# Optimization experiments

Measured on AMD Instinct MI355X. Metric: run time of the kernel, lower is better.

Reference implementation:

```python
import jax, jax.numpy as jnp
import numpy as np

B, S, D, NH = 128, 1500, 128, 4
HD = D // NH          # 32
V = 4096
K = 4                 # causal conv kernel size
FF = 192              # round_up(1.3 * 128, 64) per xLSTM FeedForwardConfig
EPS = 1e-5
NEG = -1e30           # acts as -inf for the stabilizer state


def layer_norm(x, w):
    mu = jnp.mean(x, axis=-1, keepdims=True)
    var = jnp.mean((x - mu) ** 2, axis=-1, keepdims=True)
    return (x - mu) * jax.lax.rsqrt(var + EPS) * w


def _forward(seq, emb, conv_w, conv_b, Wi, Wf, Wz, Wo, Ri, Rf, Rz, Ro,
             bi, bf, bz, bo, gn_w, ln1_w, ln2_w, ffn_up, ffn_down, ln_post_w):
    x = emb[seq]                                   # (B,S,D) embedding (row 0 = pad)
    h = layer_norm(x, ln1_w)                       # pre-norm of sLSTM block
    # causal depthwise conv + SiLU feeds the i/f gate projections
    xc = jax.lax.conv_general_dilated(
        h, conv_w, window_strides=(1,), padding=[(K - 1, 0)],
        dimension_numbers=("NWC", "WIO", "NWC"), feature_group_count=D) + conv_b
    xc = jax.nn.silu(xc)

    def headproj(v, W):                            # block-diagonal per-head linear
        return jnp.einsum("bshd,hed->bshe", v.reshape(B, S, NH, HD), W)

    gi, gf = headproj(xc, Wi), headproj(xc, Wf)
    gz, go = headproj(h, Wz), headproj(h, Wo)
    gates = jnp.stack([gi, gf, gz, go], 0).transpose(2, 0, 1, 3, 4)  # (S,4,B,NH,HD)

    def step(carry, g):
        y, c, n, m = carry                         # each (B,NH,HD)
        ir = g[0] + jnp.einsum("bhd,hde->bhe", y, Ri) + bi
        fr = g[1] + jnp.einsum("bhd,hde->bhe", y, Rf) + bf
        zr = g[2] + jnp.einsum("bhd,hde->bhe", y, Rz) + bz
        orr = g[3] + jnp.einsum("bhd,hde->bhe", y, Ro) + bo
        logf = m + jax.nn.log_sigmoid(fr)          # stabilized exponential gating
        m_new = jnp.maximum(ir, logf)
        ig = jnp.exp(ir - m_new)
        fg = jnp.exp(logf - m_new)
        c_new = fg * c + ig * jnp.tanh(zr)
        n_new = fg * n + ig
        y_new = jax.nn.sigmoid(orr) * c_new / n_new
        return (y_new, c_new, n_new, m_new), y_new

    z0 = jnp.zeros((B, NH, HD), jnp.float32)
    m0 = jnp.full((B, NH, HD), NEG, jnp.float32)
    _, ys = jax.lax.scan(step, (z0, z0, z0, m0), gates)  # (S,B,NH,HD)

    y = ys.transpose(1, 0, 2, 3)                   # (B,S,NH,HD)
    mu = jnp.mean(y, axis=-1, keepdims=True)       # multi-head group norm
    var = jnp.mean((y - mu) ** 2, axis=-1, keepdims=True)
    y = (y - mu) * jax.lax.rsqrt(var + EPS) * gn_w.reshape(NH, HD)
    x = x + y.reshape(B, S, D)                     # residual

    h2 = layer_norm(x, ln2_w)                      # gated FFN (GEGLU-style, bias-free)
    u = h2 @ ffn_up                                # (B,S,2*FF)
    x = x + (jax.nn.gelu(u[..., :FF], approximate=False) * u[..., FF:]) @ ffn_down
    x = layer_norm(x, ln_post_w)                   # post-blocks LayerNorm
    return jnp.mean(x, axis=1)                     # mean pool -> (B,D)


def setup_inputs():
    key = jax.random.key(0)
    ks = jax.random.split(key, 24)
    sc = lambda k, shp, s=0.05: jax.random.normal(k, shp, jnp.float32) * s
    emb = sc(ks[0], (V, D), 0.1).at[0].set(0.0)    # padding_idx=0
    return {
        "seq": jax.random.randint(ks[1], (B, S), 0, V),
        "emb": emb,
        "conv_w": sc(ks[2], (K, 1, D), 0.1),
        "conv_b": sc(ks[3], (D,), 0.02),
        "Wi": sc(ks[4], (NH, HD, HD), 0.1),
        "Wf": sc(ks[5], (NH, HD, HD), 0.1),
        "Wz": sc(ks[6], (NH, HD, HD), 0.1),
        "Wo": sc(ks[7], (NH, HD, HD), 0.1),
        "Ri": sc(ks[8], (NH, HD, HD), 0.1),
        "Rf": sc(ks[9], (NH, HD, HD), 0.1),
        "Rz": sc(ks[10], (NH, HD, HD), 0.1),
        "Ro": sc(ks[11], (NH, HD, HD), 0.1),
        "bi": sc(ks[12], (NH, HD), 0.02),
        "bf": jnp.tile(jnp.linspace(3.0, 6.0, HD, dtype=jnp.float32), (NH, 1)),
        "bz": sc(ks[14], (NH, HD), 0.02),
        "bo": sc(ks[15], (NH, HD), 0.02),
        "gn_w": jnp.ones((D,), jnp.float32),
        "ln1_w": jnp.ones((D,), jnp.float32),
        "ln2_w": jnp.ones((D,), jnp.float32),
        "ffn_up": sc(ks[16], (D, 2 * FF), 0.08),
        "ffn_down": sc(ks[17], (FF, D), 0.08),
        "ln_post_w": jnp.ones((D,), jnp.float32),
    }


def reference(seq, emb, conv_w, conv_b, Wi, Wf, Wz, Wo, Ri, Rf, Rz, Ro,
              bi, bf, bz, bo, gn_w, ln1_w, ln2_w, ffn_up, ffn_down, ln_post_w):
    return _forward(seq, emb, conv_w, conv_b, Wi, Wf, Wz, Wo, Ri, Rf, Rz, Ro,
                    bi, bf, bz, bo, gn_w, ln1_w, ln2_w, ffn_up, ffn_down, ln_post_w)
```

## Files before the change

kernel.cpp:

```cpp
#include <hip/hip_runtime.h>
#include <hip/hip_bf16.h>
#include <math.h>

#define BB   128
#define SS   1500
#define DD   128
#define NHH  4
#define HDD  32
#define FFF  192
#define EPSV 1e-5f
#define GXCH 16

typedef __bf16   bf16x8 __attribute__((ext_vector_type(8)));
typedef float    f32x4  __attribute__((ext_vector_type(4)));
typedef float    f32x2  __attribute__((ext_vector_type(2)));
typedef _Float16 f16x2  __attribute__((ext_vector_type(2)));

__global__ void __launch_bounds__(256) k_stats(
    const int* __restrict__ seq, const float* __restrict__ emb,
    float* __restrict__ stats)
{
    const int w = threadIdx.x >> 6, l = threadIdx.x & 63;
    for (int t = blockIdx.x * 4 + w; t < BB * SS; t += gridDim.x * 4) {
        int tok = seq[t];
        f32x2 v = *(const f32x2*)(emb + (size_t)tok * DD + 2 * l);
        float s1 = v[0] + v[1], s2 = v[0] * v[0] + v[1] * v[1];
        #pragma unroll
        for (int mm = 1; mm <= 32; mm <<= 1) {
            s1 += __shfl_xor(s1, mm);
            s2 += __shfl_xor(s2, mm);
        }
        if (l == 0) {
            float mu  = s1 * (1.f / 128.f);
            float var = s2 * (1.f / 128.f) - mu * mu;
            stats[2 * t]     = mu;
            stats[2 * t + 1] = rsqrtf(var + EPSV);
        }
    }
}

__global__ void k_prep(const float* __restrict__ up, const float* __restrict__ down,
                       const float* __restrict__ Ri, const float* __restrict__ Rf,
                       const float* __restrict__ Rz, const float* __restrict__ Ro,
                       __bf16* __restrict__ wupT, __bf16* __restrict__ wdnT,
                       float* __restrict__ rtA, float* __restrict__ rtB)
{
    int i = blockIdx.x * 256 + threadIdx.x;
    if (i < 384 * 128) {
        int n = i >> 7, k = i & 127;
        wupT[i] = (__bf16)up[k * 384 + n];
    }
    int j = i - 384 * 128;
    if (j >= 0 && j < 128 * 192) {
        int n = j / 192, k = j - n * 192;
        wdnT[j] = (__bf16)down[k * 128 + n];
    }
    int kx = i - (384 * 128 + 128 * 192);
    if (kx >= 0 && kx < 8192) {
        int h = kx >> 11, upq = (kx >> 10) & 1, e = (kx >> 5) & 31, d = kx & 31;
        int src = h * 1024 + d * 32 + e;
        rtA[kx] = upq ? Rz[src] : Ri[src];
        rtB[kx] = upq ? Ro[src] : Rf[src];
    }
}

__global__ void __launch_bounds__(256, 2) k_gx(
    const int* __restrict__ seq, const float* __restrict__ emb,
    const float* __restrict__ stats,
    const float* __restrict__ convw, const float* __restrict__ convb,
    const float* __restrict__ ln1w,
    const float* __restrict__ Wi, const float* __restrict__ Wf,
    const float* __restrict__ Wz, const float* __restrict__ Wo,
    const float* __restrict__ bi, const float* __restrict__ bfv,
    const float* __restrict__ bz, const float* __restrict__ bo,
    unsigned int* __restrict__ gx)
{
    __shared__ float hl[(GXCH + 3) * 128];
    __shared__ float xcl[4 * 32];

    const int tid = threadIdx.x;
    const int w   = tid >> 6;
    const int l   = tid & 63;
    const int p   = l >> 5;
    const int e   = l & 31;
    const int b   = blockIdx.y;
    const int s0  = blockIdx.x * GXCH;
    const int ch  = w * 32 + e;

    const float* W0 = p ? Wf : Wi;
    const float* W1 = p ? Wo : Wz;
    float wr0[32], wr1[32];
    #pragma unroll
    for (int q = 0; q < 32; ++q) {
        wr0[q] = W0[w * 1024 + e * 32 + q];
        wr1[q] = W1[w * 1024 + e * 32 + q];
    }
    #pragma unroll
    for (int q = 0; q < 32; ++q) {
        asm volatile("" : "+v"(wr0[q]));
        asm volatile("" : "+v"(wr1[q]));
    }
    const float b0 = (p ? bfv : bi)[w * 32 + e];
    const float b1 = (p ? bo  : bz)[w * 32 + e];
    const float cb = convb[ch];
    float cw[4];
    #pragma unroll
    for (int k = 0; k < 4; ++k) cw[k] = convw[k * DD + ch];

    for (int idx = tid; idx < (GXCH + 3) * 128; idx += 256) {
        int r = idx >> 7, d = idx & 127;
        int sg = s0 - 3 + r;
        float hv = 0.f;
        if (sg >= 0 && sg < SS) {
            int tok = seq[b * SS + sg];
            float mu = stats[2 * (b * SS + sg)];
            float rs = stats[2 * (b * SS + sg) + 1];
            hv = (emb[(size_t)tok * DD + d] - mu) * rs * ln1w[d];
        }
        hl[idx] = hv;
    }
    __syncthreads();

    for (int t = 0; t < GXCH; ++t) {
        if (s0 + t >= SS) break;
        float xc = cb;
        #pragma unroll
        for (int k = 0; k < 4; ++k) xc = fmaf(hl[(t + k) * 128 + ch], cw[k], xc);
        xc = xc * __builtin_amdgcn_rcpf(1.f + __expf(-xc));
        if (l < 32) xcl[w * 32 + e] = xc;

        const f32x4* xs = (const f32x4*)(xcl + w * 32);
        const f32x4* hs = (const f32x4*)(hl + (t + 3) * 128 + w * 32);

        float a0 = b0, a1 = 0.f, c0 = b1, c1 = 0.f;
        #pragma unroll
        for (int q8 = 0; q8 < 8; q8 += 2) {
            f32x4 xv0 = xs[q8], xv1 = xs[q8 + 1];
            f32x4 hv0 = hs[q8], hv1 = hs[q8 + 1];
            #pragma unroll
            for (int j = 0; j < 4; ++j) {
                a0 = fmaf(xv0[j], wr0[4 * q8 + j],     a0);
                a1 = fmaf(xv1[j], wr0[4 * q8 + 4 + j], a1);
                c0 = fmaf(hv0[j], wr1[4 * q8 + j],     c0);
                c1 = fmaf(hv1[j], wr1[4 * q8 + 4 + j], c1);
            }
        }
        float a = a0 + a1;
        float cz = c0 + c1;

        float ap = __shfl_xor(a, 32);
        float cp = __shfl_xor(cz, 32);
        if (l < 32) {
            f16x2 w0; w0[0] = (_Float16)a;  w0[1] = (_Float16)ap;
            f16x2 w1; w1[0] = (_Float16)cz; w1[1] = (_Float16)cp;
            size_t base = ((size_t)(b * 4 + w) * SS + s0 + t) * 64;
            gx[base + l]      = __builtin_bit_cast(unsigned int, w0);
            gx[base + 32 + l] = __builtin_bit_cast(unsigned int, w1);
        }
    }
}

__global__ void __launch_bounds__(64, 1)
__attribute__((amdgpu_waves_per_eu(1)))
k_scan2(
    const unsigned int* __restrict__ gx,
    const float* __restrict__ rtA, const float* __restrict__ rtB,
    _Float16* __restrict__ yout)
{
    const int l  = threadIdx.x;
    const int up = l >> 5;
    const int e  = l & 31;
    const int bh = blockIdx.x;
    const int b  = bh >> 2, h = bh & 3;

    const float* pa = rtA + ((size_t)((h * 2 + up) * 32 + e) * 32);
    const float* pb = rtB + ((size_t)((h * 2 + up) * 32 + e) * 32);
    f32x4 A0 = *(const f32x4*)(pa +  0), A1 = *(const f32x4*)(pa +  4);
    f32x4 A2 = *(const f32x4*)(pa +  8), A3 = *(const f32x4*)(pa + 12);
    f32x4 A4 = *(const f32x4*)(pa + 16), A5 = *(const f32x4*)(pa + 20);
    f32x4 A6 = *(const f32x4*)(pa + 24), A7 = *(const f32x4*)(pa + 28);
    f32x4 B0 = *(const f32x4*)(pb +  0), B1 = *(const f32x4*)(pb +  4);
    f32x4 B2 = *(const f32x4*)(pb +  8), B3 = *(const f32x4*)(pb + 12);
    f32x4 B4 = *(const f32x4*)(pb + 16), B5 = *(const f32x4*)(pb + 20);
    f32x4 B6 = *(const f32x4*)(pb + 24), B7 = *(const f32x4*)(pb + 28);
    asm volatile("" : "+v"(A0), "+v"(A1), "+v"(A2), "+v"(A3),
                      "+v"(A4), "+v"(A5), "+v"(A6), "+v"(A7),
                      "+v"(B0), "+v"(B1), "+v"(B2), "+v"(B3),
                      "+v"(B4), "+v"(B5), "+v"(B6), "+v"(B7));

    float y = 0.f, c = 0.f, n = 0.f, m = -1e30f;

    const unsigned int* gp = gx + (size_t)bh * SS * 64 + l;
    _Float16* yp = yout + (size_t)b * SS * DD + h * 32 + e;

    unsigned int pf[4];
    #pragma unroll
    for (int u = 0; u < 4; ++u) pf[u] = gp[(size_t)u * 64];

    for (int s0 = 0; s0 < SS; s0 += 4) {
        #pragma unroll
        for (int u = 0; u < 4; ++u) {
            int s = s0 + u;
            unsigned int gword = pf[u];
            int spf = (s + 4 < SS) ? s + 4 : SS - 1;
            pf[u] = gp[(size_t)spf * 64];

            f16x2 gh = __builtin_bit_cast(f16x2, gword);

            float yq[32];
            #pragma unroll
            for (int q = 0; q < 32; ++q)
                yq[q] = __builtin_bit_cast(float,
                          __builtin_amdgcn_readlane(__builtin_bit_cast(int, y), q));

            float a0 = (float)gh[0], a1 = 0.f, a2 = 0.f, a3 = 0.f;
            float c0 = (float)gh[1], c1 = 0.f, c2 = 0.f, c3 = 0.f;
            #pragma unroll
            for (int j = 0; j < 4; ++j) {
                a0 = fmaf(yq[j],      A0[j], a0);
                a0 = fmaf(yq[4 + j],  A1[j], a0);
                a1 = fmaf(yq[8 + j],  A2[j], a1);
                a1 = fmaf(yq[12 + j], A3[j], a1);
                a2 = fmaf(yq[16 + j], A4[j], a2);
                a2 = fmaf(yq[20 + j], A5[j], a2);
                a3 = fmaf(yq[24 + j], A6[j], a3);
                a3 = fmaf(yq[28 + j], A7[j], a3);
                c0 = fmaf(yq[j],      B0[j], c0);
                c0 = fmaf(yq[4 + j],  B1[j], c0);
                c1 = fmaf(yq[8 + j],  B2[j], c1);
                c1 = fmaf(yq[12 + j], B3[j], c1);
                c2 = fmaf(yq[16 + j], B4[j], c2);
                c2 = fmaf(yq[20 + j], B5[j], c2);
                c3 = fmaf(yq[24 + j], B6[j], c3);
                c3 = fmaf(yq[28 + j], B7[j], c3);
            }
            float accA = (a0 + a1) + (a2 + a3);
            float accB = (c0 + c1) + (c2 + c3);

            float zr  = __shfl_xor(accA, 32);
            float orr = __shfl_xor(accB, 32);
            float ir  = accA, fr = accB;

            float lsig = fminf(fr, 0.f) - __logf(1.f + __expf(-fabsf(fr)));
            float lf   = m + lsig;
            float mn   = fmaxf(ir, lf);
            float ig   = __expf(ir - mn);
            float fg   = __expf(lf - mn);
            float e2   = __expf(2.f * zr);
            float zt   = 1.f - 2.f * __builtin_amdgcn_rcpf(e2 + 1.f);
            c = fg * c + ig * zt;
            n = fg * n + ig;
            float so = __builtin_amdgcn_rcpf(1.f + __expf(-orr));
            y = so * c * __builtin_amdgcn_rcpf(n);
            m = mn;

            if (!up) yp[(size_t)s * DD] = (_Float16)y;
        }
    }
}

__global__ void __launch_bounds__(64) k_scan_fused(
    const int* __restrict__ seq, const float* __restrict__ emb,
    const float* __restrict__ stats,
    const float* __restrict__ convw, const float* __restrict__ convb,
    const float* __restrict__ ln1w,
    const float* __restrict__ Wi, const float* __restrict__ Wf,
    const float* __restrict__ Wz, const float* __restrict__ Wo,
    const float* __restrict__ Ri, const float* __restrict__ Rf,
    const float* __restrict__ Rz, const float* __restrict__ Ro,
    const float* __restrict__ bi, const float* __restrict__ bfv,
    const float* __restrict__ bz, const float* __restrict__ bo,
    _Float16* __restrict__ yout)
{
    __shared__ int   stok[SS];
    __shared__ float smu[SS];
    __shared__ float srs[SS];

    const int lane = threadIdx.x;
    const int half = lane >> 5;
    const int e    = lane & 31;
    const int d0   = half * 16;
    const int bh   = blockIdx.x;
    const int b    = bh >> 2, h = bh & 3;
    const int ch   = h * 32 + e;

    for (int i = lane; i < SS; i += 64) {
        stok[i] = seq[b * SS + i];
        f32x2 st = *(const f32x2*)(stats + (size_t)(b * SS + i) * 2);
        smu[i] = st[0];
        srs[i] = st[1];
    }
    __syncthreads();

    float wi[16], wf[16], wz[16], wo[16];
    float ri[16], rf[16], rz[16], ro[16];
    {
        const float* Wib = Wi + h * 1024 + e * 32 + d0;
        const float* Wfb = Wf + h * 1024 + e * 32 + d0;
        const float* Wzb = Wz + h * 1024 + e * 32 + d0;
        const float* Wob = Wo + h * 1024 + e * 32 + d0;
        const float* Rib = Ri + h * 1024 + d0 * 32 + e;
        const float* Rfb = Rf + h * 1024 + d0 * 32 + e;
        const float* Rzb = Rz + h * 1024 + d0 * 32 + e;
        const float* Rob = Ro + h * 1024 + d0 * 32 + e;
        #pragma unroll
        for (int q = 0; q < 16; ++q) {
            wi[q] = Wib[q]; wf[q] = Wfb[q]; wz[q] = Wzb[q]; wo[q] = Wob[q];
            ri[q] = Rib[q * 32]; rf[q] = Rfb[q * 32];
            rz[q] = Rzb[q * 32]; ro[q] = Rob[q * 32];
        }
    }
    const float biv = bi [h * 32 + e];
    const float bfb = bfv[h * 32 + e];
    const float bzv = bz [h * 32 + e];
    const float bov = bo [h * 32 + e];
    const float lnv = ln1w[ch];
    const float cbr = convb[ch];
    const float cw0 = convw[0 * DD + ch], cw1 = convw[1 * DD + ch];
    const float cw2 = convw[2 * DD + ch], cw3 = convw[3 * DD + ch];

    float y = 0.f, c = 0.f, n = 0.f, m = -1e30f;
    float hm1 = 0.f, hm2 = 0.f, hm3 = 0.f;

    _Float16* yp = yout + ((size_t)b * SS) * DD + ch;

    float x0 = emb[(size_t)stok[0] * DD + ch];
    float x1 = (SS > 1) ? emb[(size_t)stok[1] * DD + ch] : 0.f;

    for (int s = 0; s < SS; ++s) {
        float x2 = 0.f;
        if (s + 2 < SS) x2 = emb[(size_t)stok[s + 2] * DD + ch];

        float h0 = (x0 - smu[s]) * srs[s] * lnv;
        float xc = cbr;
        xc = fmaf(hm3, cw0, xc);
        xc = fmaf(hm2, cw1, xc);
        xc = fmaf(hm1, cw2, xc);
        xc = fmaf(h0,  cw3, xc);
        xc = xc / (1.f + __expf(-xc));
        hm3 = hm2; hm2 = hm1; hm1 = h0;

        float ir = 0.f, fr = 0.f, zr = 0.f, orr = 0.f;
        #pragma unroll
        for (int q = 0; q < 16; ++q) {
            float xd = __shfl(xc, d0 + q, 32);
            float hd = __shfl(h0, d0 + q, 32);
            float yd = __shfl(y,  d0 + q, 32);
            ir  = fmaf(xd, wi[q], ir);
            fr  = fmaf(xd, wf[q], fr);
            zr  = fmaf(hd, wz[q], zr);
            orr = fmaf(hd, wo[q], orr);
            ir  = fmaf(yd, ri[q], ir);
            fr  = fmaf(yd, rf[q], fr);
            zr  = fmaf(yd, rz[q], zr);
            orr = fmaf(yd, ro[q], orr);
        }
        ir  += __shfl_xor(ir, 32);
        fr  += __shfl_xor(fr, 32);
        zr  += __shfl_xor(zr, 32);
        orr += __shfl_xor(orr, 32);
        ir += biv; fr += bfb; zr += bzv; orr += bov;

        float lsig = fminf(fr, 0.f) - __logf(1.f + __expf(-fabsf(fr)));
        float lf   = m + lsig;
        float mn   = fmaxf(ir, lf);
        float ig   = __expf(ir - mn);
        float fg   = __expf(lf - mn);
        float e2   = __expf(2.f * zr);
        float zt   = 1.f - 2.f / (e2 + 1.f);
        c = fg * c + ig * zt;
        n = fg * n + ig;
        float so = 1.f / (1.f + __expf(-orr));
        y = so * c / n;
        m = mn;

        if (half == 0) yp[(size_t)s * DD] = (_Float16)y;
        x0 = x1; x1 = x2;
    }
}

__global__ void __launch_bounds__(256) k_ffn(
    const int* __restrict__ seq, const float* __restrict__ emb,
    const _Float16* __restrict__ yb, const float* __restrict__ gnw,
    const float* __restrict__ ln2w, const float* __restrict__ lnpw,
    const __bf16* __restrict__ wupT, const __bf16* __restrict__ wdnT,
    float* __restrict__ out)
{
    __shared__ __bf16 h2l[32 * 136];
    __shared__ __bf16 fl [32 * 200];
    __shared__ float  xrl[32 * 132];

    const int tid = threadIdx.x;
    const int w   = tid >> 6, l = tid & 63;
    const int lr  = l & 15,  lh = l >> 4;
    const int b   = blockIdx.y;
    const int t0  = blockIdx.x * 32;

    const float gw0 = gnw[2 * l],  gw1 = gnw[2 * l + 1];
    const float l2w0 = ln2w[2 * l], l2w1 = ln2w[2 * l + 1];
    const float lpw0 = lnpw[2 * l], lpw1 = lnpw[2 * l + 1];

    for (int it = 0; it < 8; ++it) {
        int tt = it * 4 + w;
        int stok = t0 + tt;
        float x0 = 0.f, x1 = 0.f, y0 = 0.f, y1 = 0.f;
        if (stok < SS) {
            int tk = seq[b * SS + stok];
            f32x2 xv = *(const f32x2*)(emb + (size_t)tk * DD + 2 * l);
            f16x2 yv = *(const f16x2*)(yb + ((size_t)b * SS + stok) * DD + 2 * l);
            x0 = xv[0]; x1 = xv[1]; y0 = (float)yv[0]; y1 = (float)yv[1];
        }
        float s1 = y0 + y1, s2 = y0 * y0 + y1 * y1;
        #pragma unroll
        for (int mm = 1; mm <= 8; mm <<= 1) { s1 += __shfl_xor(s1, mm); s2 += __shfl_xor(s2, mm); }
        float mu  = s1 * (1.f / 32.f);
        float var = s2 * (1.f / 32.f) - mu * mu;
        float inv = rsqrtf(var + EPSV);
        float xr0 = x0 + (y0 - mu) * inv * gw0;
        float xr1 = x1 + (y1 - mu) * inv * gw1;
        float t1 = xr0 + xr1, t2 = xr0 * xr0 + xr1 * xr1;
        #pragma unroll
        for (int mm = 1; mm <= 32; mm <<= 1) { t1 += __shfl_xor(t1, mm); t2 += __shfl_xor(t2, mm); }
        float mu2  = t1 * (1.f / 128.f);
        float var2 = t2 * (1.f / 128.f) - mu2 * mu2;
        float inv2 = rsqrtf(var2 + EPSV);
        xrl[tt * 132 + 2 * l]     = xr0;
        xrl[tt * 132 + 2 * l + 1] = xr1;
        h2l[tt * 136 + 2 * l]     = (__bf16)((xr0 - mu2) * inv2 * l2w0);
        h2l[tt * 136 + 2 * l + 1] = (__bf16)((xr1 - mu2) * inv2 * l2w1);
    }
    __syncthreads();

    f32x4 acc1[2][6];
    #pragma unroll
    for (int mt = 0; mt < 2; ++mt)
        #pragma unroll
        for (int nt = 0; nt < 6; ++nt)
            acc1[mt][nt] = (f32x4){0.f, 0.f, 0.f, 0.f};

    #pragma unroll
    for (int kk = 0; kk < 4; ++kk) {
        int k0 = kk * 32;
        bf16x8 bfr[6];
        #pragma unroll
        for (int nt = 0; nt < 6; ++nt) {
            int colbase = (nt < 3) ? (w * 48 + nt * 16) : (192 + w * 48 + (nt - 3) * 16);
            bfr[nt] = *(const bf16x8*)(wupT + (colbase + lr) * DD + k0 + lh * 8);
        }
        #pragma unroll
        for (int mt = 0; mt < 2; ++mt) {
            bf16x8 afr = *(const bf16x8*)(h2l + (mt * 16 + lr) * 136 + k0 + lh * 8);
            #pragma unroll
            for (int nt = 0; nt < 6; ++nt)
                acc1[mt][nt] = __builtin_amdgcn_mfma_f32_16x16x32_bf16(afr, bfr[nt], acc1[mt][nt], 0, 0, 0);
        }
    }

    #pragma unroll
    for (int mt = 0; mt < 2; ++mt)
        #pragma unroll
        for (int nt = 0; nt < 3; ++nt)
            #pragma unroll
            for (int j = 0; j < 4; ++j) {
                int r = mt * 16 + lh * 4 + j;
                int cN = w * 48 + nt * 16 + lr;
                float a  = acc1[mt][nt][j];
                float bv = acc1[mt][nt + 3][j];
                float ge = 0.5f * a * (1.f + erff(a * 0.70710678118f));
                fl[r * 200 + cN] = (__bf16)(ge * bv);
            }
    __syncthreads();

    f32x4 acc2[2][2];
    #pragma unroll
    for (int mt = 0; mt < 2; ++mt) {
        acc2[mt][0] = (f32x4){0.f, 0.f, 0.f, 0.f};
        acc2[mt][1] = (f32x4){0.f, 0.f, 0.f, 0.f};
    }
    #pragma unroll
    for (int kk = 0; kk < 6; ++kk) {
        int k0 = kk * 32;
        bf16x8 bfr2[2];
        #pragma unroll
        for (int nt = 0; nt < 2; ++nt)
            bfr2[nt] = *(const bf16x8*)(wdnT + (w * 32 + nt * 16 + lr) * FFF + k0 + lh * 8);
        #pragma unroll
        for (int mt = 0; mt < 2; ++mt) {
            bf16x8 afr = *(const bf16x8*)(fl + (mt * 16 + lr) * 200 + k0 + lh * 8);
            #pragma unroll
            for (int nt = 0; nt < 2; ++nt)
                acc2[mt][nt] = __builtin_amdgcn_mfma_f32_16x16x32_bf16(afr, bfr2[nt], acc2[mt][nt], 0, 0, 0);
        }
    }
    #pragma unroll
    for (int mt = 0; mt < 2; ++mt)
        #pragma unroll
        for (int nt = 0; nt < 2; ++nt)
            #pragma unroll
            for (int j = 0; j < 4; ++j) {
                int r  = mt * 16 + lh * 4 + j;
                int cN = w * 32 + nt * 16 + lr;
                xrl[r * 132 + cN] += acc2[mt][nt][j];
            }
    __syncthreads();

    float p0 = 0.f, p1 = 0.f;
    for (int it = 0; it < 8; ++it) {
        int tt = it * 4 + w;
        int stok = t0 + tt;
        if (stok >= SS) continue;
        float xr0 = xrl[tt * 132 + 2 * l];
        float xr1 = xrl[tt * 132 + 2 * l + 1];
        float t1 = xr0 + xr1, t2 = xr0 * xr0 + xr1 * xr1;
        #pragma unroll
        for (int mm = 1; mm <= 32; mm <<= 1) { t1 += __shfl_xor(t1, mm); t2 += __shfl_xor(t2, mm); }
        float mu  = t1 * (1.f / 128.f);
        float var = t2 * (1.f / 128.f) - mu * mu;
        float inv = rsqrtf(var + EPSV);
        p0 += (xr0 - mu) * inv * lpw0;
        p1 += (xr1 - mu) * inv * lpw1;
    }
    atomicAdd(out + b * DD + 2 * l,     p0 * (1.f / SS));
    atomicAdd(out + b * DD + 2 * l + 1, p1 * (1.f / SS));
}

extern "C" void kernel_launch(void* const* d_in, const int* in_sizes, int n_in,
                              void* d_out, int out_size, void* d_ws, size_t ws_size,
                              hipStream_t stream)
{
    const int*   seq   = (const int*)  d_in[0];
    const float* emb   = (const float*)d_in[1];
    const float* convw = (const float*)d_in[2];
    const float* convb = (const float*)d_in[3];
    const float* Wi    = (const float*)d_in[4];
    const float* Wf    = (const float*)d_in[5];
    const float* Wz    = (const float*)d_in[6];
    const float* Wo    = (const float*)d_in[7];
    const float* Ri    = (const float*)d_in[8];
    const float* Rf    = (const float*)d_in[9];
    const float* Rz    = (const float*)d_in[10];
    const float* Ro    = (const float*)d_in[11];
    const float* bi    = (const float*)d_in[12];
    const float* bfp   = (const float*)d_in[13];
    const float* bz    = (const float*)d_in[14];
    const float* bo    = (const float*)d_in[15];
    const float* gnw   = (const float*)d_in[16];
    const float* ln1w  = (const float*)d_in[17];
    const float* ln2w  = (const float*)d_in[18];
    const float* ffup  = (const float*)d_in[19];
    const float* ffdn  = (const float*)d_in[20];
    const float* lnpw  = (const float*)d_in[21];
    float* out = (float*)d_out;

    char* ws = (char*)d_ws;
    float*        stats = (float*)ws;
    _Float16*     yws   = (_Float16*)(ws + 1536000);
    __bf16*       wupT  = (__bf16*)(ws + 50688000);
    __bf16*       wdnT  = (__bf16*)(ws + 50786304);
    float*        rtA   = (float*)(ws + 50835456);
    float*        rtB   = (float*)(ws + 50868224);
    unsigned int* gxb   = (unsigned int*)(ws + 50900992);
    const size_t NEED_GX = 50900992ull + 196608000ull;

    hipMemsetAsync(d_out, 0, (size_t)BB * DD * sizeof(float), stream);

    hipLaunchKernelGGL(k_stats, dim3(2048), dim3(256), 0, stream, seq, emb, stats);
    hipLaunchKernelGGL(k_prep, dim3(320), dim3(256), 0, stream,
                       ffup, ffdn, Ri, Rf, Rz, Ro, wupT, wdnT, rtA, rtB);

    if (ws_size >= NEED_GX) {
        hipLaunchKernelGGL(k_gx, dim3((SS + GXCH - 1) / GXCH, BB), dim3(256), 0, stream,
                           seq, emb, stats, convw, convb, ln1w,
                           Wi, Wf, Wz, Wo, bi, bfp, bz, bo, gxb);
        hipLaunchKernelGGL(k_scan2, dim3(512), dim3(64), 0, stream,
                           gxb, rtA, rtB, yws);
    } else {
        hipLaunchKernelGGL(k_scan_fused, dim3(512), dim3(64), 0, stream,
                           seq, emb, stats, convw, convb, ln1w,
                           Wi, Wf, Wz, Wo, Ri, Rf, Rz, Ro, bi, bfp, bz, bo, yws);
    }
    hipLaunchKernelGGL(k_ffn, dim3(47, 128), dim3(256), 0, stream,
                       seq, emb, yws, gnw, ln2w, lnpw, wupT, wdnT, out);
}
```

Before: 992.4 us.

## Interleave two independent scan chains per wavefront in sLSTM scan kernel

The recurrent scan kernel now processes two (batch, head) chains per 64-lane wavefront, stepping them alternately so their serial dependency chains can overlap, and the grid is halved from 512 to 256 blocks. Both half-waves now compute all four gate values and store y, instead of only the lower half storing. This trades parallelism across waves and SIMDs for instruction-level parallelism inside one wave. It doubles the recurrent-weight register footprint and leaves fewer waves in flight, so it could run slower if two waves on separate SIMDs were already overlapping well.

```diff
diff --git a/kernel.cpp b/kernel.cpp
--- a/kernel.cpp
+++ b/kernel.cpp
@@ -160,6 +160,50 @@
     }
 }
 
+#define SCAN_STEP(GW, A0,A1,A2,A3,A4,A5,A6,A7, B0,B1,B2,B3,B4,B5,B6,B7, Y, C, N, M, YP, S) \
+{                                                                              \
+    f16x2 gh = __builtin_bit_cast(f16x2, GW);                                  \
+    float yq[32];                                                              \
+    _Pragma("unroll")                                                          \
+    for (int q = 0; q < 32; ++q)                                               \
+        yq[q] = __builtin_bit_cast(float,                                      \
+                  __builtin_amdgcn_readlane(__builtin_bit_cast(int, Y), q));   \
+    float a0 = (float)gh[0], a1 = 0.f, a2 = 0.f, a3 = 0.f;                     \
+    float c0 = (float)gh[1], c1 = 0.f, c2 = 0.f, c3 = 0.f;                     \
+    _Pragma("unroll")                                                          \
+    for (int j = 0; j < 4; ++j) {                                              \
+        a0 = fmaf(yq[j],      A0[j], a0);  a0 = fmaf(yq[4 + j],  A1[j], a0);   \
+        a1 = fmaf(yq[8 + j],  A2[j], a1);  a1 = fmaf(yq[12 + j], A3[j], a1);   \
+        a2 = fmaf(yq[16 + j], A4[j], a2);  a2 = fmaf(yq[20 + j], A5[j], a2);   \
+        a3 = fmaf(yq[24 + j], A6[j], a3);  a3 = fmaf(yq[28 + j], A7[j], a3);   \
+        c0 = fmaf(yq[j],      B0[j], c0);  c0 = fmaf(yq[4 + j],  B1[j], c0);   \
+        c1 = fmaf(yq[8 + j],  B2[j], c1);  c1 = fmaf(yq[12 + j], B3[j], c1);   \
+        c2 = fmaf(yq[16 + j], B4[j], c2);  c2 = fmaf(yq[20 + j], B5[j], c2);   \
+        c3 = fmaf(yq[24 + j], B6[j], c3);  c3 = fmaf(yq[28 + j], B7[j], c3);   \
+    }                                                                          \
+    float accA = (a0 + a1) + (a2 + a3);                                        \
+    float accB = (c0 + c1) + (c2 + c3);                                        \
+    float crA = __shfl_xor(accA, 32);                                          \
+    float crB = __shfl_xor(accB, 32);                                          \
+    float ir  = up ? crA  : accA;                                              \
+    float fr  = up ? crB  : accB;                                              \
+    float zr  = up ? accA : crA;                                               \
+    float orr = up ? accB : crB;                                               \
+    float lsig = fminf(fr, 0.f) - __logf(1.f + __expf(-fabsf(fr)));            \
+    float lf = M + lsig;                                                       \
+    float mn = fmaxf(ir, lf);                                                  \
+    float ig = __expf(ir - mn);                                                \
+    float fg = __expf(lf - mn);                                                \
+    float e2 = __expf(2.f * zr);                                               \
+    float zt = 1.f - 2.f * __builtin_amdgcn_rcpf(e2 + 1.f);                    \
+    C = fg * C + ig * zt;                                                      \
+    N = fg * N + ig;                                                           \
+    float so = __builtin_amdgcn_rcpf(1.f + __expf(-orr));                      \
+    Y = so * C * __builtin_amdgcn_rcpf(N);                                     \
+    M = mn;                                                                    \
+    YP[(size_t)(S) * DD] = (_Float16)Y;                                        \
+}
+
 __global__ void __launch_bounds__(64, 1)
 __attribute__((amdgpu_waves_per_eu(1)))
 k_scan2(
@@ -170,91 +214,71 @@
     const int l  = threadIdx.x;
     const int up = l >> 5;
     const int e  = l & 31;
-    const int bh = blockIdx.x;
-    const int b  = bh >> 2, h = bh & 3;
-
-    const float* pa = rtA + ((size_t)((h * 2 + up) * 32 + e) * 32);
-    const float* pb = rtB + ((size_t)((h * 2 + up) * 32 + e) * 32);
-    f32x4 A0 = *(const f32x4*)(pa +  0), A1 = *(const f32x4*)(pa +  4);
-    f32x4 A2 = *(const f32x4*)(pa +  8), A3 = *(const f32x4*)(pa + 12);
-    f32x4 A4 = *(const f32x4*)(pa + 16), A5 = *(const f32x4*)(pa + 20);
-    f32x4 A6 = *(const f32x4*)(pa + 24), A7 = *(const f32x4*)(pa + 28);
-    f32x4 B0 = *(const f32x4*)(pb +  0), B1 = *(const f32x4*)(pb +  4);
-    f32x4 B2 = *(const f32x4*)(pb +  8), B3 = *(const f32x4*)(pb + 12);
-    f32x4 B4 = *(const f32x4*)(pb + 16), B5 = *(const f32x4*)(pb + 20);
-    f32x4 B6 = *(const f32x4*)(pb + 24), B7 = *(const f32x4*)(pb + 28);
-    asm volatile("" : "+v"(A0), "+v"(A1), "+v"(A2), "+v"(A3),
-                      "+v"(A4), "+v"(A5), "+v"(A6), "+v"(A7),
-                      "+v"(B0), "+v"(B1), "+v"(B2), "+v"(B3),
-                      "+v"(B4), "+v"(B5), "+v"(B6), "+v"(B7));
-
-    float y = 0.f, c = 0.f, n = 0.f, m = -1e30f;
-
-    const unsigned int* gp = gx + (size_t)bh * SS * 64 + l;
-    _Float16* yp = yout + (size_t)b * SS * DD + h * 32 + e;
-
-    unsigned int pf[4];
-    #pragma unroll
-    for (int u = 0; u < 4; ++u) pf[u] = gp[(size_t)u * 64];
+    const int chA = blockIdx.x * 2;
+    const int chB = chA + 1;
+    const int bA = chA >> 2, hA = chA & 3;
+    const int bB = chB >> 2, hB = chB & 3;
+
+    const float* paA = rtA + ((size_t)((hA * 2 + up) * 32 + e) * 32);
+    const float* pbA = rtB + ((size_t)((hA * 2 + up) * 32 + e) * 32);
+    const float* paB = rtA + ((size_t)((hB * 2 + up) * 32 + e) * 32);
+    const float* pbB = rtB + ((size_t)((hB * 2 + up) * 32 + e) * 32);
+
+    f32x4 RA0 = *(const f32x4*)(paA +  0), RA1 = *(const f32x4*)(paA +  4);
+    f32x4 RA2 = *(const f32x4*)(paA +  8), RA3 = *(const f32x4*)(paA + 12);
+    f32x4 RA4 = *(const f32x4*)(paA + 16), RA5 = *(const f32x4*)(paA + 20);
+    f32x4 RA6 = *(const f32x4*)(paA + 24), RA7 = *(const f32x4*)(paA + 28);
+    f32x4 SA0 = *(const f32x4*)(pbA +  0), SA1 = *(const f32x4*)(pbA +  4);
+    f32x4 SA2 = *(const f32x4*)(pbA +  8), SA3 = *(const f32x4*)(pbA + 12);
+    f32x4 SA4 = *(const f32x4*)(pbA + 16), SA5 = *(const f32x4*)(pbA + 20);
+    f32x4 SA6 = *(const f32x4*)(pbA + 24), SA7 = *(const f32x4*)(pbA + 28);
+    f32x4 RB0 = *(const f32x4*)(paB +  0), RB1 = *(const f32x4*)(paB +  4);
+    f32x4 RB2 = *(const f32x4*)(paB +  8), RB3 = *(const f32x4*)(paB + 12);
+    f32x4 RB4 = *(const f32x4*)(paB + 16), RB5 = *(const f32x4*)(paB + 20);
+    f32x4 RB6 = *(const f32x4*)(paB + 24), RB7 = *(const f32x4*)(paB + 28);
+    f32x4 SB0 = *(const f32x4*)(pbB +  0), SB1 = *(const f32x4*)(pbB +  4);
+    f32x4 SB2 = *(const f32x4*)(pbB +  8), SB3 = *(const f32x4*)(pbB + 12);
+    f32x4 SB4 = *(const f32x4*)(pbB + 16), SB5 = *(const f32x4*)(pbB + 20);
+    f32x4 SB6 = *(const f32x4*)(pbB + 24), SB7 = *(const f32x4*)(pbB + 28);
+    asm volatile("" : "+v"(RA0), "+v"(RA1), "+v"(RA2), "+v"(RA3),
+                      "+v"(RA4), "+v"(RA5), "+v"(RA6), "+v"(RA7),
+                      "+v"(SA0), "+v"(SA1), "+v"(SA2), "+v"(SA3),
+                      "+v"(SA4), "+v"(SA5), "+v"(SA6), "+v"(SA7));
+    asm volatile("" : "+v"(RB0), "+v"(RB1), "+v"(RB2), "+v"(RB3),
+                      "+v"(RB4), "+v"(RB5), "+v"(RB6), "+v"(RB7),
+                      "+v"(SB0), "+v"(SB1), "+v"(SB2), "+v"(SB3),
+                      "+v"(SB4), "+v"(SB5), "+v"(SB6), "+v"(SB7));
+
+    float yA = 0.f, cA = 0.f, nA = 0.f, mA = -1e30f;
+    float yB = 0.f, cB = 0.f, nB = 0.f, mB = -1e30f;
+
+    const unsigned int* gpA = gx + (size_t)chA * SS * 64 + l;
+    const unsigned int* gpB = gx + (size_t)chB * SS * 64 + l;
+    _Float16* ypA = yout + (size_t)bA * SS * DD + hA * 32 + e;
+    _Float16* ypB = yout + (size_t)bB * SS * DD + hB * 32 + e;
+
+    unsigned int pfA[4], pfB[4];
+    #pragma unroll
+    for (int u = 0; u < 4; ++u) {
+        pfA[u] = gpA[(size_t)u * 64];
+        pfB[u] = gpB[(size_t)u * 64];
+    }
 
     for (int s0 = 0; s0 < SS; s0 += 4) {
         #pragma unroll
         for (int u = 0; u < 4; ++u) {
             int s = s0 + u;
-            unsigned int gword = pf[u];
+            unsigned int gA = pfA[u], gB = pfB[u];
             int spf = (s + 4 < SS) ? s + 4 : SS - 1;
-            pf[u] = gp[(size_t)spf * 64];
-
-            f16x2 gh = __builtin_bit_cast(f16x2, gword);
-
-            float yq[32];
-            #pragma unroll
-            for (int q = 0; q < 32; ++q)
-                yq[q] = __builtin_bit_cast(float,
-                          __builtin_amdgcn_readlane(__builtin_bit_cast(int, y), q));
-
-            float a0 = (float)gh[0], a1 = 0.f, a2 = 0.f, a3 = 0.f;
-            float c0 = (float)gh[1], c1 = 0.f, c2 = 0.f, c3 = 0.f;
-            #pragma unroll
-            for (int j = 0; j < 4; ++j) {
-                a0 = fmaf(yq[j],      A0[j], a0);
-                a0 = fmaf(yq[4 + j],  A1[j], a0);
-                a1 = fmaf(yq[8 + j],  A2[j], a1);
-                a1 = fmaf(yq[12 + j], A3[j], a1);
-                a2 = fmaf(yq[16 + j], A4[j], a2);
-                a2 = fmaf(yq[20 + j], A5[j], a2);
-                a3 = fmaf(yq[24 + j], A6[j], a3);
-                a3 = fmaf(yq[28 + j], A7[j], a3);
-                c0 = fmaf(yq[j],      B0[j], c0);
-                c0 = fmaf(yq[4 + j],  B1[j], c0);
-                c1 = fmaf(yq[8 + j],  B2[j], c1);
-                c1 = fmaf(yq[12 + j], B3[j], c1);
-                c2 = fmaf(yq[16 + j], B4[j], c2);
-                c2 = fmaf(yq[20 + j], B5[j], c2);
-                c3 = fmaf(yq[24 + j], B6[j], c3);
-                c3 = fmaf(yq[28 + j], B7[j], c3);
-            }
-            float accA = (a0 + a1) + (a2 + a3);
-            float accB = (c0 + c1) + (c2 + c3);
-
-            float zr  = __shfl_xor(accA, 32);
-            float orr = __shfl_xor(accB, 32);
-            float ir  = accA, fr = accB;
-
-            float lsig = fminf(fr, 0.f) - __logf(1.f + __expf(-fabsf(fr)));
-            float lf   = m + lsig;
-            float mn   = fmaxf(ir, lf);
-            float ig   = __expf(ir - mn);
-            float fg   = __expf(lf - mn);
-            float e2   = __expf(2.f * zr);
-            float zt   = 1.f - 2.f * __builtin_amdgcn_rcpf(e2 + 1.f);
-            c = fg * c + ig * zt;
-            n = fg * n + ig;
-            float so = __builtin_amdgcn_rcpf(1.f + __expf(-orr));
-            y = so * c * __builtin_amdgcn_rcpf(n);
-            m = mn;
-
-            if (!up) yp[(size_t)s * DD] = (_Float16)y;
+            pfA[u] = gpA[(size_t)spf * 64];
+            pfB[u] = gpB[(size_t)spf * 64];
+
+            SCAN_STEP(gA, RA0,RA1,RA2,RA3,RA4,RA5,RA6,RA7,
+                          SA0,SA1,SA2,SA3,SA4,SA5,SA6,SA7,
+                          yA, cA, nA, mA, ypA, s);
+            SCAN_STEP(gB, RB0,RB1,RB2,RB3,RB4,RB5,RB6,RB7,
+                          SB0,SB1,SB2,SB3,SB4,SB5,SB6,SB7,
+                          yB, cB, nB, mB, ypB, s);
         }
     }
 }
@@ -572,7 +596,7 @@
         hipLaunchKernelGGL(k_gx, dim3((SS + GXCH - 1) / GXCH, BB), dim3(256), 0, stream,
                            seq, emb, stats, convw, convb, ln1w,
                            Wi, Wf, Wz, Wo, bi, bfp, bz, bo, gxb);
-        hipLaunchKernelGGL(k_scan2, dim3(512), dim3(64), 0, stream,
+        hipLaunchKernelGGL(k_scan2, dim3(256), dim3(64), 0, stream,
                            gxb, rtA, rtB, yws);
     } else {
         hipLaunchKernelGGL(k_scan_fused, dim3(512), dim3(64), 0, stream,
```

Measured after the change: 1.325 ms. 33.5% more time.
